# Optimization experiments

Measured on AMD Instinct MI355X. Metric: run time of the kernel, lower is better.

## Reference

```python
import jax, jax.numpy as jnp
import numpy as np
import math

B, A, T = 64, 23, 128          # batch, num_agents, max seq len
D, AE, S, H = 256, 32, 6, 8    # d_model, agent_encoding_dim, static_dim, heads
DK = D // H                     # 32
DM = D + AE                     # 288, MHA q/k/v dim
NEG = -1e10                     # masked_fill constant from source


def sinusoidal_pe(pos, d):
    # pos: int array [...], returns [..., d] standard transformer PE at positions pos
    half = jnp.arange(d // 2, dtype=jnp.float32)
    div = jnp.exp(-half * (math.log(10000.0) * 2.0 / d))          # [d/2]
    ang = pos[..., None].astype(jnp.float32) * div                # [..., d/2]
    return jnp.stack([jnp.sin(ang), jnp.cos(ang)], axis=-1).reshape(*pos.shape, d)


def setup_inputs() -> dict:
    key = jax.random.key(0)
    ks = jax.random.split(key, 20)
    std = 0.02
    data = jax.random.normal(ks[0], (B, A, T), jnp.float32)
    lengths = jax.random.randint(ks[1], (B, A), 0, T + 1).astype(jnp.int32)   # mask arg = lengths
    t = jnp.arange(T, dtype=jnp.int32)
    time = jnp.where(t[None, None, :] < lengths[:, :, None], t[None, None, :], -1)  # [B,A,T], -1 = pad
    static = jax.random.normal(ks[2], (B, S), jnp.float32)
    # per-agent Linear(1, D): weight [A, D], bias [A, D]
    W_embed = std * jax.random.normal(ks[3], (A, D), jnp.float32)
    b_embed = std * jax.random.normal(ks[4], (A, D), jnp.float32)
    E_var = std * jax.random.normal(ks[5], (A, AE), jnp.float32)            # VariateEncoding table
    W_static = std * jax.random.normal(ks[6], (S, D), jnp.float32)
    b_static = jnp.zeros((D,), jnp.float32)
    Wq = std * jax.random.normal(ks[7], (DM, D), jnp.float32); bq = jnp.zeros((D,), jnp.float32)
    Wk = std * jax.random.normal(ks[8], (DM, D), jnp.float32); bk = jnp.zeros((D,), jnp.float32)
    Wv = std * jax.random.normal(ks[9], (DM, D), jnp.float32); bv = jnp.zeros((D,), jnp.float32)
    Wo = std * jax.random.normal(ks[10], (D, DM), jnp.float32); bo = jnp.zeros((DM,), jnp.float32)
    Wg = std * jax.random.normal(ks[11], (DM + D, 1), jnp.float32); bg = jnp.zeros((1,), jnp.float32)
    return dict(data=data, time=time, mask=lengths, static=static,
                W_embed=W_embed, b_embed=b_embed, E_var=E_var,
                W_static=W_static, b_static=b_static,
                Wq=Wq, bq=bq, Wk=Wk, bk=bk, Wv=Wv, bv=bv, Wo=Wo, bo=bo,
                Wg=Wg, bg=bg)


def reference(data, time, mask, static, W_embed, b_embed, E_var, W_static, b_static,
              Wq, bq, Wk, bk, Wv, bv, Wo, bo, Wg, bg):
    lengths = mask                                            # [B,A] sequence lengths
    t = jnp.arange(T)
    valid = t[None, None, :] < lengths[:, :, None]            # [B,A,T] bool
    # mask_matrix[i,:len,:len]=1 double loop -> vectorized outer product
    mask4 = valid[:, :, :, None] & valid[:, :, None, :]       # [B,A,T,T]

    # per-agent Linear(1, D) loop -> batched rank-1 affine, then ReLU
    data_embeds = jax.nn.relu(data[..., None] * W_embed[None, :, None, :]
                              + b_embed[None, :, None, :])    # [B,A,T,D]

    # src_pe: sinusoidal positional encoding at (clamped) time values
    pe = sinusoidal_pe(jnp.maximum(time, 0), D)               # [B,A,T,D]
    src = data_embeds + pe

    # variate (agent-id) embedding concat -> [B,A,T,D+AE]; encoder = identity
    var = jnp.broadcast_to(E_var[None, :, None, :], (B, A, T, AE))
    memory = jnp.concatenate([src, var], axis=-1)             # [B,A,T,DM]

    # time-masked mean pool over T
    time_mask = time >= 0                                     # [B,A,T]
    memory = jnp.where(time_mask[..., None], memory, 0.0)
    counts = time_mask.sum(axis=2).astype(memory.dtype)       # [B,A]
    agentwise = memory.sum(axis=2) / (counts[..., None] + 1e-9)  # [B,A,DM]

    # custom MHA (dim='Time'): q_len = 1 per agent, keys/values over T
    q = jnp.einsum('bae,ed->bad', agentwise, Wq) + bq          # [B,A,D]
    k = jnp.einsum('bate,ed->batd', memory, Wk) + bk           # [B,A,T,D]
    v = jnp.einsum('bate,ed->batd', memory, Wv) + bv
    qh = q.reshape(B, A, H, DK)                                # [B,A,H,DK] (q_len=1 squeezed)
    kh = k.reshape(B, A, T, H, DK).transpose(0, 1, 3, 2, 4)    # [B,A,H,T,DK]
    vh = v.reshape(B, A, T, H, DK).transpose(0, 1, 3, 2, 4)
    scores = jnp.einsum('bahd,bahtd->baht', qh, kh) / math.sqrt(DK)  # [B,A,H,T]
    amask = mask4[:, :, 0, :]                                  # [B,A,T] row 0 of per-agent mask
    scores = jnp.where(amask[:, :, None, :], scores, NEG)
    p = jax.nn.softmax(scores, axis=-1)                        # dropout = eval (identity)
    ctx = jnp.einsum('baht,bahtd->bahd', p, vh).reshape(B, A, D)
    agent_feat = jnp.einsum('bad,de->bae', ctx, Wo) + bo       # [B,A,DM]

    # agent-masked mean pool over agents
    agent_mask = counts > 0                                    # [B,A]
    agent_feat = jnp.where(agent_mask[..., None], agent_feat, 0.0)
    denom = agent_mask.sum(axis=1).astype(agent_feat.dtype) + 1e-9
    aggre = agent_feat.sum(axis=1) / denom[:, None]            # [B,DM]

    static_feat = static @ W_static + b_static                 # [B,D]
    all_feature = jnp.concatenate([aggre, static_feat], axis=-1)  # [B,DM+D]
    return all_feature @ Wg + bg                               # [B,1]


if __name__ == '__main__':
    out = reference(**setup_inputs())
    print(out.shape, jnp.asarray(out).dtype)
```

## Files before the change

### kernel.cpp

```cpp
#include <hip/hip_runtime.h>
#include <math.h>

#define NB 64
#define NA 23
#define NT 128
#define ND 256
#define NAE 32
#define NS 6
#define NH 8
#define NDM 288

#define OFF_PEK    0
#define OFF_PECUM  32768
#define OFF_WKT    65536
#define OFF_VWO    131072
#define OFF_PEMV   133120
#define OFF_EVA    134144
#define OFF_CST    134328
#define OFF_SB     134336

__global__ __launch_bounds__(256) void setup1_kernel(
    const float* __restrict__ Wk, const float* __restrict__ Wv,
    const float* __restrict__ Wo, const float* __restrict__ Wg,
    const float* __restrict__ bv, const float* __restrict__ bo,
    const float* __restrict__ W_static, const float* __restrict__ b_static,
    const float* __restrict__ bg, const float* __restrict__ E_var,
    float* __restrict__ ws)
{
    const int blk = blockIdx.x;
    const int tid = threadIdx.x;
    float* PEcum = ws + OFF_PECUM;
    float* WkT   = ws + OFF_WKT;
    float* VWo   = ws + OFF_VWO;
    float* cst   = ws + OFF_CST;

    if (blk < 128) {
        const int g = tid >> 7, t = tid & 127;
        const int e = blk * 2 + g;
        const int i = e >> 1;
        const float kdiv = 0.07195578415606394f;
        const float dv = expf(-(float)i * kdiv);
        const float ang = (float)t * dv;
        const float v = (e & 1) ? cosf(ang) : sinf(ang);
        __shared__ float buf[256];
        buf[tid] = v;
        #pragma unroll
        for (int s = 1; s < 128; s <<= 1) {
            __syncthreads();
            float add = (t >= s) ? buf[tid - s] : 0.f;
            __syncthreads();
            buf[tid] += add;
        }
        __syncthreads();
        PEcum[t * ND + e] = buf[tid];
    } else if (blk < 384) {
        const int j = blk - 128;
        const float scale = 0.17677669529663687f;
        WkT[j * 256 + tid] = Wk[tid * ND + j] * scale;
    } else if (blk < 392) {
        const int h = blk - 384;
        __shared__ float wog[32];
        __shared__ float vext[32];
        __shared__ float vbS;
        {
            const int jj = tid >> 3, sub = tid & 7;
            const int j = h * 32 + jj;
            float acc = 0.f;
            const int m0 = sub * 36;
            #pragma unroll 4
            for (int m = m0; m < m0 + 36; ++m)
                acc = fmaf(Wo[j * NDM + m], Wg[m], acc);
            acc += __shfl_down(acc, 4, 8);
            acc += __shfl_down(acc, 2, 8);
            acc += __shfl_down(acc, 1, 8);
            if (sub == 0) wog[jj] = acc;
        }
        __syncthreads();
        {
            float acc = 0.f;
            #pragma unroll 8
            for (int jj = 0; jj < 32; ++jj)
                acc = fmaf(Wv[tid * ND + h * 32 + jj], wog[jj], acc);
            VWo[h * 256 + tid] = acc;
        }
        if (tid < 32) {
            float acc = 0.f;
            #pragma unroll 8
            for (int jj = 0; jj < 32; ++jj)
                acc = fmaf(Wv[(256 + tid) * ND + h * 32 + jj], wog[jj], acc);
            vext[tid] = acc;
        }
        if (tid == 0) {
            float acc = 0.f;
            #pragma unroll 8
            for (int jj = 0; jj < 32; ++jj)
                acc = fmaf(bv[h * 32 + jj], wog[jj], acc);
            vbS = acc;
        }
        __syncthreads();
        if (tid < NA) {
            float acc = vbS;
            #pragma unroll 8
            for (int ee = 0; ee < 32; ++ee)
                acc = fmaf(E_var[tid * NAE + ee], vext[ee], acc);
            ws[OFF_EVA + tid * NH + h] = acc;
        }
    } else {
        const int i = tid >> 5, sub = tid & 31;
        float acc = 0.f;
        if (i < 6) {
            for (int m = sub; m < 256; m += 32)
                acc = fmaf(W_static[i * ND + m], Wg[NDM + m], acc);
        } else if (i == 6) {
            for (int m = sub; m < 256; m += 32)
                acc = fmaf(b_static[m], Wg[NDM + m], acc);
        } else {
            for (int m = sub; m < NDM; m += 32)
                acc = fmaf(bo[m], Wg[m], acc);
        }
        #pragma unroll
        for (int off = 16; off > 0; off >>= 1)
            acc += __shfl_down(acc, off, 32);
        if (sub == 0) cst[i] = (i == 6) ? acc + bg[0] : acc;
    }
}

__global__ __launch_bounds__(256) void setup2_kernel(
    const float* __restrict__ Wk, float* __restrict__ ws)
{
    const int t = blockIdx.x;
    const int tid = threadIdx.x;
    __shared__ float peS[256];
    {
        const int i = tid >> 1;
        const float kdiv = 0.07195578415606394f;
        const float dv = expf(-(float)i * kdiv);
        const float ang = (float)t * dv;
        peS[tid] = (tid & 1) ? cosf(ang) : sinf(ang);
    }
    __syncthreads();
    {
        float a0 = 0.f, a1 = 0.f, a2 = 0.f, a3 = 0.f;
        #pragma unroll 4
        for (int e = 0; e < 256; e += 4) {
            a0 = fmaf(peS[e],     Wk[ e      * ND + tid], a0);
            a1 = fmaf(peS[e + 1], Wk[(e + 1) * ND + tid], a1);
            a2 = fmaf(peS[e + 2], Wk[(e + 2) * ND + tid], a2);
            a3 = fmaf(peS[e + 3], Wk[(e + 3) * ND + tid], a3);
        }
        const float scale = 0.17677669529663687f;
        ws[OFF_PEK + tid * NT + t] = ((a0 + a1) + (a2 + a3)) * scale;
    }
    {
        const int h = tid >> 5, ee = tid & 31;
        const float* vw = ws + OFF_VWO + h * 256;
        float v = 0.f;
        #pragma unroll
        for (int k = 0; k < 8; ++k)
            v = fmaf(peS[ee + 32 * k], vw[ee + 32 * k], v);
        v += __shfl_down(v, 16, 32);
        v += __shfl_down(v, 8, 32);
        v += __shfl_down(v, 4, 32);
        v += __shfl_down(v, 2, 32);
        v += __shfl_down(v, 1, 32);
        if (ee == 0) ws[OFF_PEMV + h * NT + t] = v;
    }
    if (t == 0 && tid < NB) ws[OFF_SB + tid] = 0.f;
}

#define E_ITER(KCNT) do {                                                    \
    const int e = ebase + ee;                                                \
    const int r = (e + (e >> 6)) & 3;                                        \
    const float2 wb = Wb[half][e + (e >> 6)];                                \
    const float4 cq = comboV[e * 4 + (hh ^ r)];                              \
    const float4 cm = comboV[e * 4 + ((2 | hh) ^ r)];                        \
    const float m0 = fmaxf(fmaf(xt0, wb.x, wb.y), 0.f);                      \
    aS[0][0]=fmaf(m0,cq.x,aS[0][0]); aS[0][1]=fmaf(m0,cq.y,aS[0][1]);        \
    aS[0][2]=fmaf(m0,cq.z,aS[0][2]); aS[0][3]=fmaf(m0,cq.w,aS[0][3]);        \
    aM[0][0]=fmaf(m0,cm.x,aM[0][0]); aM[0][1]=fmaf(m0,cm.y,aM[0][1]);        \
    aM[0][2]=fmaf(m0,cm.z,aM[0][2]); aM[0][3]=fmaf(m0,cm.w,aM[0][3]);        \
    const float m1 = fmaxf(fmaf(xt1, wb.x, wb.y), 0.f);                      \
    aS[1][0]=fmaf(m1,cq.x,aS[1][0]); aS[1][1]=fmaf(m1,cq.y,aS[1][1]);        \
    aS[1][2]=fmaf(m1,cq.z,aS[1][2]); aS[1][3]=fmaf(m1,cq.w,aS[1][3]);        \
    aM[1][0]=fmaf(m1,cm.x,aM[1][0]); aM[1][1]=fmaf(m1,cm.y,aM[1][1]);        \
    aM[1][2]=fmaf(m1,cm.z,aM[1][2]); aM[1][3]=fmaf(m1,cm.w,aM[1][3]);        \
    if ((KCNT) == 4) {                                                       \
        const float m2 = fmaxf(fmaf(xt2, wb.x, wb.y), 0.f);                  \
        aS[2][0]=fmaf(m2,cq.x,aS[2][0]); aS[2][1]=fmaf(m2,cq.y,aS[2][1]);    \
        aS[2][2]=fmaf(m2,cq.z,aS[2][2]); aS[2][3]=fmaf(m2,cq.w,aS[2][3]);    \
        aM[2][0]=fmaf(m2,cm.x,aM[2][0]); aM[2][1]=fmaf(m2,cm.y,aM[2][1]);    \
        aM[2][2]=fmaf(m2,cm.z,aM[2][2]); aM[2][3]=fmaf(m2,cm.w,aM[2][3]);    \
        const float m3 = fmaxf(fmaf(xt3, wb.x, wb.y), 0.f);                  \
        aS[3][0]=fmaf(m3,cq.x,aS[3][0]); aS[3][1]=fmaf(m3,cq.y,aS[3][1]);    \
        aS[3][2]=fmaf(m3,cq.z,aS[3][2]); aS[3][3]=fmaf(m3,cq.w,aS[3][3]);    \
        aM[3][0]=fmaf(m3,cm.x,aM[3][0]); aM[3][1]=fmaf(m3,cm.y,aM[3][1]);    \
        aM[3][2]=fmaf(m3,cm.z,aM[3][2]); aM[3][3]=fmaf(m3,cm.w,aM[3][3]);    \
    }                                                                        \
} while (0)

__global__ __launch_bounds__(512) void main_kernel(
    const float* __restrict__ data, const int* __restrict__ lengths,
    const float* __restrict__ W_embed, const float* __restrict__ b_embed,
    const float* __restrict__ E_var,
    const float* __restrict__ Wq, const float* __restrict__ bq,
    float* __restrict__ ws)
{
    const int pair = blockIdx.x;
    const int tid  = threadIdx.x;
    const int half = tid >> 8;
    const int lt   = tid & 255;
    const int wgh  = pair * 2 + half;
    const int ah   = wgh % NA;
    const int bh   = wgh / NA;
    const int Lh   = lengths[wgh];

    __shared__ __align__(16) float xs[2][NT];
    __shared__ __align__(16) float qs[2][ND];
    __shared__ float2 Wb[2][ND + 4];
    __shared__ __align__(16) float combo[2][ND * 16];
    __shared__ float red[2][4];

    const float* PEcum = ws + OFF_PECUM;
    const float* WkT   = ws + OFF_WKT;
    const float* VWo   = ws + OFF_VWO;
    const float* cstp  = ws + OFF_CST;
    float* agA = &combo[1][0];

    if (lt < NT) xs[half][lt] = data[wgh * NT + lt];
    __syncthreads();
    {
        const int e = lt;
        if (Lh > 0) {
            const float We = W_embed[ah * ND + e];
            const float be = b_embed[ah * ND + e];
            Wb[half][e + (e >> 6)] = make_float2(We, be);
            const float4* x4 = (const float4*)xs[half];
            float s0 = 0.f, s1 = 0.f, s2 = 0.f, s3 = 0.f;
            const int nq = Lh >> 2;
            for (int q = 0; q < nq; ++q) {
                const float4 xv = x4[q];
                s0 += fmaxf(fmaf(xv.x, We, be), 0.f);
                s1 += fmaxf(fmaf(xv.y, We, be), 0.f);
                s2 += fmaxf(fmaf(xv.z, We, be), 0.f);
                s3 += fmaxf(fmaf(xv.w, We, be), 0.f);
            }
            for (int t = nq * 4; t < Lh; ++t)
                s0 += fmaxf(fmaf(xs[half][t], We, be), 0.f);
            agA[half * NDM + e] = (((s0 + s1) + (s2 + s3)) + PEcum[(Lh - 1) * ND + e]) / (float)Lh;
        } else {
            Wb[half][e + (e >> 6)] = make_float2(0.f, 0.f);
            agA[half * NDM + e] = 0.f;
        }
    }
    if (lt < NAE) agA[half * NDM + ND + lt] = (Lh > 0) ? E_var[ah * NAE + lt] : 0.f;
    __syncthreads();

    {
        const int j = lt;
        const float4* a40 = (const float4*)(agA);
        const float4* a41 = (const float4*)(agA + NDM);
        const int fi0 = half * 36;
        float c0 = 0.f, c1 = 0.f, c2 = 0.f, c3 = 0.f;
        #pragma unroll 4
        for (int fi = fi0; fi < fi0 + 36; ++fi) {
            const float4 av0 = a40[fi];
            const float4 av1 = a41[fi];
            const int f = fi * 4;
            const float w0 = Wq[ f      * ND + j];
            const float w1 = Wq[(f + 1) * ND + j];
            const float w2 = Wq[(f + 2) * ND + j];
            const float w3 = Wq[(f + 3) * ND + j];
            c0 = fmaf(av0.x, w0, c0); c2 = fmaf(av0.y, w1, c2);
            c0 = fmaf(av0.z, w2, c0); c2 = fmaf(av0.w, w3, c2);
            c1 = fmaf(av1.x, w0, c1); c3 = fmaf(av1.y, w1, c3);
            c1 = fmaf(av1.z, w2, c1); c3 = fmaf(av1.w, w3, c3);
        }
        float* Csc = &combo[0][0];
        Csc[half * 512 +       j] = c0 + c2;
        Csc[half * 512 + 256 + j] = c1 + c3;
    }
    __syncthreads();
    {
        const float* Csc = &combo[0][0];
        qs[half][lt] = bq[lt] + Csc[half * 256 + lt] + Csc[512 + half * 256 + lt];
    }
    __syncthreads();

    {
        const int e = lt;
        const int hb = half;
        const float* wr = WkT + (hb * 128) * 256 + e;
        const float4* q40 = (const float4*)(qs[0] + hb * 128);
        const float4* q41 = (const float4*)(qs[1] + hb * 128);
        float qk0[4], qk1[4];
        #pragma unroll
        for (int h4 = 0; h4 < 4; ++h4) {
            float c00 = 0.f, c01 = 0.f, c10 = 0.f, c11 = 0.f;
            #pragma unroll
            for (int jq = 0; jq < 8; ++jq) {
                const float4 q0 = q40[h4 * 8 + jq];
                const float4 q1 = q41[h4 * 8 + jq];
                const float w0 = wr[(h4 * 32 + jq * 4 + 0) * 256];
                const float w1 = wr[(h4 * 32 + jq * 4 + 1) * 256];
                const float w2 = wr[(h4 * 32 + jq * 4 + 2) * 256];
                const float w3 = wr[(h4 * 32 + jq * 4 + 3) * 256];
                c00 = fmaf(w0, q0.x, c00); c01 = fmaf(w1, q0.y, c01);
                c00 = fmaf(w2, q0.z, c00); c01 = fmaf(w3, q0.w, c01);
                c10 = fmaf(w0, q1.x, c10); c11 = fmaf(w1, q1.y, c11);
                c10 = fmaf(w2, q1.z, c10); c11 = fmaf(w3, q1.w, c11);
            }
            qk0[h4] = c00 + c01;
            qk1[h4] = c10 + c11;
        }
        const int r = (e + (e >> 6)) & 3;
        float4* row0 = (float4*)(&combo[0][0]) + e * 4;
        float4* row1 = (float4*)(&combo[1][0]) + e * 4;
        row0[hb ^ r] = make_float4(qk0[0], qk0[1], qk0[2], qk0[3]);
        row1[hb ^ r] = make_float4(qk1[0], qk1[1], qk1[2], qk1[3]);
        const float4 vw = make_float4(VWo[(hb * 4 + 0) * 256 + e],
                                      VWo[(hb * 4 + 1) * 256 + e],
                                      VWo[(hb * 4 + 2) * 256 + e],
                                      VWo[(hb * 4 + 3) * 256 + e]);
        row0[(2 | hb) ^ r] = vw;
        row1[(2 | hb) ^ r] = vw;
    }
    __syncthreads();

    {
        const int lane = lt & 63;
        const int wv   = lt >> 6;
        const int hh   = wv & 1;
        const int tw   = wv >> 1;
        const int t0   = lane & 15;
        const int c    = lane >> 4;
        const int tb   = tw * 16 + t0;
        const int ebase = c * 64;
        const float4* comboV = (const float4*)(&combo[half][0]);
        float aS[4][4], aM[4][4];
        #pragma unroll
        for (int k = 0; k < 4; ++k)
            #pragma unroll
            for (int j = 0; j < 4; ++j) { aS[k][j] = 0.f; aM[k][j] = 0.f; }
        const float xt0 = xs[half][tb];
        const float xt1 = xs[half][tb + 32];
        const float xt2 = xs[half][tb + 64];
        const float xt3 = xs[half][tb + 96];
        if (Lh > 64) {
            #pragma unroll 4
            for (int ee = 0; ee < 64; ++ee) E_ITER(4);
        } else if (Lh > 0) {
            #pragma unroll 4
            for (int ee = 0; ee < 64; ++ee) E_ITER(2);
        }
        #pragma unroll
        for (int k = 0; k < 4; ++k)
            #pragma unroll
            for (int j = 0; j < 4; ++j) {
                float vS = aS[k][j], vM = aM[k][j];
                vS += __shfl_down(vS, 32, 64);
                vS += __shfl_down(vS, 16, 64);
                vM += __shfl_down(vM, 32, 64);
                vM += __shfl_down(vM, 16, 64);
                aS[k][j] = vS; aM[k][j] = vM;
            }
        __syncthreads();
        float* scF = &combo[half][0];
        float* mvF = scF + 1024;
        if (c == 0) {
            #pragma unroll
            for (int k = 0; k < 4; ++k)
                #pragma unroll
                for (int j = 0; j < 4; ++j) {
                    const int h = hh * 4 + j;
                    scF[h * NT + tb + 32 * k] = aS[k][j];
                    mvF[h * NT + tb + 32 * k] = aM[k][j];
                }
        }
    }
    __syncthreads();

    {
        const int h  = tid >> 6;
        const int tq = tid & 63;
        const float* pekt = ws + OFF_PEK;
        const float4* qs40 = (const float4*)(qs[0] + h * 32);
        const float4* qs41 = (const float4*)(qs[1] + h * 32);
        float b00 = 0.f, b01 = 0.f, b10 = 0.f, b11 = 0.f;
        #pragma unroll
        for (int jq = 0; jq < 8; ++jq) {
            const float4 q0 = qs40[jq];
            const float4 q1 = qs41[jq];
            const float* pr = pekt + (h * 32 + jq * 4) * NT + tq;
            const float p00 = pr[0];          const float p01 = pr[64];
            const float p10 = pr[NT];         const float p11 = pr[NT + 64];
            const float p20 = pr[2 * NT];     const float p21 = pr[2 * NT + 64];
            const float p30 = pr[3 * NT];     const float p31 = pr[3 * NT + 64];
            b00 = fmaf(q0.x, p00, b00); b00 = fmaf(q0.y, p10, b00);
            b00 = fmaf(q0.z, p20, b00); b00 = fmaf(q0.w, p30, b00);
            b01 = fmaf(q0.x, p01, b01); b01 = fmaf(q0.y, p11, b01);
            b01 = fmaf(q0.z, p21, b01); b01 = fmaf(q0.w, p31, b01);
            b10 = fmaf(q1.x, p00, b10); b10 = fmaf(q1.y, p10, b10);
            b10 = fmaf(q1.z, p20, b10); b10 = fmaf(q1.w, p30, b10);
            b11 = fmaf(q1.x, p01, b11); b11 = fmaf(q1.y, p11, b11);
            b11 = fmaf(q1.z, p21, b11); b11 = fmaf(q1.w, p31, b11);
        }
        combo[0][2048 + h * NT + tq]      = b00;
        combo[0][2048 + h * NT + tq + 64] = b01;
        combo[1][2048 + h * NT + tq]      = b10;
        combo[1][2048 + h * NT + tq + 64] = b11;
    }
    __syncthreads();

    if (Lh > 0) {
        const float* sc   = &combo[half][0];
        const float* mvb  = sc + 1024;
        const float* qkxp = sc + 2048;
        const float* pemv = ws + OFF_PEMV;
        const int wv = lt >> 6, lane = lt & 63;
        float wsum = 0.f;
        for (int hh2 = 0; hh2 < 2; ++hh2) {
            const int h = wv * 2 + hh2;
            float s1 = (lane < Lh) ? sc[h * NT + lane] + qkxp[h * NT + lane] : -3e38f;
            float s2 = (lane + 64 < Lh) ? sc[h * NT + 64 + lane] + qkxp[h * NT + 64 + lane] : -3e38f;
            float mx = fmaxf(s1, s2);
            #pragma unroll
            for (int off = 32; off > 0; off >>= 1)
                mx = fmaxf(mx, __shfl_down(mx, off, 64));
            mx = __shfl(mx, 0, 64);
            const float vbv = ws[OFF_EVA + ah * NH + h];
            float e1 = (lane < Lh) ? __expf(s1 - mx) : 0.f;
            float e2 = (lane + 64 < Lh) ? __expf(s2 - mx) : 0.f;
            float num = e1 * (mvb[h * NT + lane] + pemv[h * NT + lane] + vbv);
            num = fmaf(e2, mvb[h * NT + 64 + lane] + pemv[h * NT + 64 + lane] + vbv, num);
            float den = e1 + e2;
            #pragma unroll
            for (int off = 32; off > 0; off >>= 1) {
                num += __shfl_down(num, off, 64);
                den += __shfl_down(den, off, 64);
            }
            if (lane == 0) wsum += num / den;
        }
        if (lane == 0) red[half][wv] = wsum;
    }
    __syncthreads();
    if (lt == 0 && Lh > 0)
        atomicAdd(ws + OFF_SB + bh,
                  cstp[7] + red[half][0] + red[half][1] + red[half][2] + red[half][3]);
}

__global__ __launch_bounds__(64) void final_kernel(
    const float* __restrict__ statics, const int* __restrict__ lengths,
    const float* __restrict__ ws, float* __restrict__ out)
{
    const int b = threadIdx.x;
    const float* cst = ws + OFF_CST;
    int n = 0;
    for (int a = 0; a < NA; ++a)
        if (lengths[b * NA + a] > 0) ++n;
    float o = ws[OFF_SB + b] / ((float)n + 1e-9f);
    #pragma unroll
    for (int i = 0; i < NS; ++i)
        o = fmaf(statics[b * NS + i], cst[i], o);
    o += cst[6];
    out[b] = o;
}

extern "C" void kernel_launch(void* const* d_in, const int* in_sizes, int n_in,
                              void* d_out, int out_size, void* d_ws, size_t ws_size,
                              hipStream_t stream) {
    const float* data     = (const float*)d_in[0];
    const int*   mask     = (const int*)d_in[2];
    const float* statics  = (const float*)d_in[3];
    const float* W_embed  = (const float*)d_in[4];
    const float* b_embed  = (const float*)d_in[5];
    const float* E_var    = (const float*)d_in[6];
    const float* W_static = (const float*)d_in[7];
    const float* b_static = (const float*)d_in[8];
    const float* Wq       = (const float*)d_in[9];
    const float* bq       = (const float*)d_in[10];
    const float* Wk       = (const float*)d_in[11];
    const float* Wv       = (const float*)d_in[13];
    const float* bv       = (const float*)d_in[14];
    const float* Wo       = (const float*)d_in[15];
    const float* bo       = (const float*)d_in[16];
    const float* Wg       = (const float*)d_in[17];
    const float* bg       = (const float*)d_in[18];
    float* out = (float*)d_out;
    float* ws  = (float*)d_ws;

    setup1_kernel<<<dim3(393), dim3(256), 0, stream>>>(Wk, Wv, Wo, Wg, bv, bo,
                                                       W_static, b_static, bg, E_var, ws);
    setup2_kernel<<<dim3(128), dim3(256), 0, stream>>>(Wk, ws);
    main_kernel<<<dim3(NB * NA / 2), dim3(512), 0, stream>>>(data, mask, W_embed, b_embed,
                                                             E_var, Wq, bq, ws);
    final_kernel<<<dim3(1), dim3(64), 0, stream>>>(statics, mask, ws, out);
}
```

Before: 151.4 us.

## Fold setup2 and final kernels into setup and main to cut launches

Moves the PE·Wk and PE·VWo projections into the transpose and VWo blocks of the first setup kernel, recomputing sin/cos per block, so the second setup kernel is removed. The final reduction kernel is replaced by a last-block-done pattern: an atomic counter in the workspace picks the last main-kernel block, which computes the output. This removes two kernel launches and their serialization gaps. In exchange it adds redundant transcendental work in setup blocks and an extra atomic plus fence per main block.

```diff
diff --git a/kernel.cpp b/kernel.cpp
--- a/kernel.cpp
+++ b/kernel.cpp
@@ -9,6 +9,7 @@
 #define NS 6
 #define NH 8
 #define NDM 288
+#define NPAIR 736
 
 #define OFF_PEK    0
 #define OFF_PECUM  32768
@@ -18,8 +19,9 @@
 #define OFF_EVA    134144
 #define OFF_CST    134328
 #define OFF_SB     134336
-
-__global__ __launch_bounds__(256) void setup1_kernel(
+#define OFF_CNT    134400
+
+__global__ __launch_bounds__(256) void setup_kernel(
     const float* __restrict__ Wk, const float* __restrict__ Wv,
     const float* __restrict__ Wo, const float* __restrict__ Wg,
     const float* __restrict__ bv, const float* __restrict__ bo,
@@ -29,6 +31,7 @@
 {
     const int blk = blockIdx.x;
     const int tid = threadIdx.x;
+    const float kdiv = 0.07195578415606394f;
     float* PEcum = ws + OFF_PECUM;
     float* WkT   = ws + OFF_WKT;
     float* VWo   = ws + OFF_VWO;
@@ -38,7 +41,6 @@
         const int g = tid >> 7, t = tid & 127;
         const int e = blk * 2 + g;
         const int i = e >> 1;
-        const float kdiv = 0.07195578415606394f;
         const float dv = expf(-(float)i * kdiv);
         const float ang = (float)t * dv;
         const float v = (e & 1) ? cosf(ang) : sinf(ang);
@@ -56,12 +58,36 @@
     } else if (blk < 384) {
         const int j = blk - 128;
         const float scale = 0.17677669529663687f;
-        WkT[j * 256 + tid] = Wk[tid * ND + j] * scale;
+        __shared__ float wkS[256];
+        __shared__ float dvS[128];
+        __shared__ float pp[256];
+        const float w = Wk[tid * ND + j] * scale;
+        WkT[j * 256 + tid] = w;
+        wkS[tid] = w;
+        if (tid < 128) dvS[tid] = expf(-(float)tid * kdiv);
+        __syncthreads();
+        {
+            const int t = tid & 127, eh = tid >> 7;
+            const float tf = (float)t;
+            float acc = 0.f;
+            const int i0 = eh * 64;
+            for (int i = i0; i < i0 + 64; ++i) {
+                const float ang = tf * dvS[i];
+                acc = fmaf(sinf(ang), wkS[2 * i],     acc);
+                acc = fmaf(cosf(ang), wkS[2 * i + 1], acc);
+            }
+            pp[tid] = acc;
+        }
+        __syncthreads();
+        if (tid < 128) ws[OFF_PEK + j * NT + tid] = pp[tid] + pp[128 + tid];
     } else if (blk < 392) {
         const int h = blk - 384;
         __shared__ float wog[32];
         __shared__ float vext[32];
         __shared__ float vbS;
+        __shared__ float vS[256];
+        __shared__ float dvS2[128];
+        __shared__ float pp2[256];
         {
             const int jj = tid >> 3, sub = tid & 7;
             const int j = h * 32 + jj;
@@ -82,15 +108,18 @@
             for (int jj = 0; jj < 32; ++jj)
                 acc = fmaf(Wv[tid * ND + h * 32 + jj], wog[jj], acc);
             VWo[h * 256 + tid] = acc;
-        }
-        if (tid < 32) {
+            vS[tid] = acc;
+        }
+        if (tid < 128) dvS2[tid] = expf(-(float)tid * kdiv);
+        if (tid >= 128 && tid < 160) {
+            const int ee = tid - 128;
             float acc = 0.f;
             #pragma unroll 8
             for (int jj = 0; jj < 32; ++jj)
-                acc = fmaf(Wv[(256 + tid) * ND + h * 32 + jj], wog[jj], acc);
-            vext[tid] = acc;
-        }
-        if (tid == 0) {
+                acc = fmaf(Wv[(256 + ee) * ND + h * 32 + jj], wog[jj], acc);
+            vext[ee] = acc;
+        }
+        if (tid == 160) {
             float acc = 0.f;
             #pragma unroll 8
             for (int jj = 0; jj < 32; ++jj)
@@ -105,7 +134,23 @@
                 acc = fmaf(E_var[tid * NAE + ee], vext[ee], acc);
             ws[OFF_EVA + tid * NH + h] = acc;
         }
+        {
+            const int t = tid & 127, eh = tid >> 7;
+            const float tf = (float)t;
+            float acc = 0.f;
+            const int i0 = eh * 64;
+            for (int i = i0; i < i0 + 64; ++i) {
+                const float ang = tf * dvS2[i];
+                acc = fmaf(sinf(ang), vS[2 * i],     acc);
+                acc = fmaf(cosf(ang), vS[2 * i + 1], acc);
+            }
+            pp2[tid] = acc;
+        }
+        __syncthreads();
+        if (tid < 128) ws[OFF_PEMV + h * NT + tid] = pp2[tid] + pp2[128 + tid];
     } else {
+        if (tid < NB) ws[OFF_SB + tid] = 0.f;
+        if (tid == NB) ws[OFF_CNT] = 0.f;
         const int i = tid >> 5, sub = tid & 31;
         float acc = 0.f;
         if (i < 6) {
@@ -123,49 +168,6 @@
             acc += __shfl_down(acc, off, 32);
         if (sub == 0) cst[i] = (i == 6) ? acc + bg[0] : acc;
     }
-}
-
-__global__ __launch_bounds__(256) void setup2_kernel(
-    const float* __restrict__ Wk, float* __restrict__ ws)
-{
-    const int t = blockIdx.x;
-    const int tid = threadIdx.x;
-    __shared__ float peS[256];
-    {
-        const int i = tid >> 1;
-        const float kdiv = 0.07195578415606394f;
-        const float dv = expf(-(float)i * kdiv);
-        const float ang = (float)t * dv;
-        peS[tid] = (tid & 1) ? cosf(ang) : sinf(ang);
-    }
-    __syncthreads();
-    {
-        float a0 = 0.f, a1 = 0.f, a2 = 0.f, a3 = 0.f;
-        #pragma unroll 4
-        for (int e = 0; e < 256; e += 4) {
-            a0 = fmaf(peS[e],     Wk[ e      * ND + tid], a0);
-            a1 = fmaf(peS[e + 1], Wk[(e + 1) * ND + tid], a1);
-            a2 = fmaf(peS[e + 2], Wk[(e + 2) * ND + tid], a2);
-            a3 = fmaf(peS[e + 3], Wk[(e + 3) * ND + tid], a3);
-        }
-        const float scale = 0.17677669529663687f;
-        ws[OFF_PEK + tid * NT + t] = ((a0 + a1) + (a2 + a3)) * scale;
-    }
-    {
-        const int h = tid >> 5, ee = tid & 31;
-        const float* vw = ws + OFF_VWO + h * 256;
-        float v = 0.f;
-        #pragma unroll
-        for (int k = 0; k < 8; ++k)
-            v = fmaf(peS[ee + 32 * k], vw[ee + 32 * k], v);
-        v += __shfl_down(v, 16, 32);
-        v += __shfl_down(v, 8, 32);
-        v += __shfl_down(v, 4, 32);
-        v += __shfl_down(v, 2, 32);
-        v += __shfl_down(v, 1, 32);
-        if (ee == 0) ws[OFF_PEMV + h * NT + t] = v;
-    }
-    if (t == 0 && tid < NB) ws[OFF_SB + tid] = 0.f;
 }
 
 #define E_ITER(KCNT) do {                                                    \
@@ -203,6 +205,7 @@
     const float* __restrict__ W_embed, const float* __restrict__ b_embed,
     const float* __restrict__ E_var,
     const float* __restrict__ Wq, const float* __restrict__ bq,
+    const float* __restrict__ statics, float* __restrict__ out,
     float* __restrict__ ws)
 {
     const int pair = blockIdx.x;
@@ -219,6 +222,7 @@
     __shared__ float2 Wb[2][ND + 4];
     __shared__ __align__(16) float combo[2][ND * 16];
     __shared__ float red[2][4];
+    __shared__ int lastFin;
 
     const float* PEcum = ws + OFF_PECUM;
     const float* WkT   = ws + OFF_WKT;
@@ -443,26 +447,31 @@
         if (lane == 0) red[half][wv] = wsum;
     }
     __syncthreads();
-    if (lt == 0 && Lh > 0)
-        atomicAdd(ws + OFF_SB + bh,
-                  cstp[7] + red[half][0] + red[half][1] + red[half][2] + red[half][3]);
-}
-
-__global__ __launch_bounds__(64) void final_kernel(
-    const float* __restrict__ statics, const int* __restrict__ lengths,
-    const float* __restrict__ ws, float* __restrict__ out)
-{
-    const int b = threadIdx.x;
-    const float* cst = ws + OFF_CST;
-    int n = 0;
-    for (int a = 0; a < NA; ++a)
-        if (lengths[b * NA + a] > 0) ++n;
-    float o = ws[OFF_SB + b] / ((float)n + 1e-9f);
-    #pragma unroll
-    for (int i = 0; i < NS; ++i)
-        o = fmaf(statics[b * NS + i], cst[i], o);
-    o += cst[6];
-    out[b] = o;
+    if (lt == 0) {
+        if (Lh > 0)
+            atomicAdd(ws + OFF_SB + bh,
+                      cstp[7] + red[half][0] + red[half][1] + red[half][2] + red[half][3]);
+        __threadfence();
+    }
+    __syncthreads();
+    if (tid == 0) {
+        const int prev = atomicAdd((int*)(ws + OFF_CNT), 1);
+        lastFin = (prev == NPAIR - 1) ? 1 : 0;
+    }
+    __syncthreads();
+    if (lastFin && tid < NB) {
+        const int b = tid;
+        const float sum = atomicAdd(ws + OFF_SB + b, 0.f);
+        int n = 0;
+        for (int a = 0; a < NA; ++a)
+            if (lengths[b * NA + a] > 0) ++n;
+        float o = sum / ((float)n + 1e-9f);
+        #pragma unroll
+        for (int i = 0; i < NS; ++i)
+            o = fmaf(statics[b * NS + i], cstp[i], o);
+        o += cstp[6];
+        out[b] = o;
+    }
 }
 
 extern "C" void kernel_launch(void* const* d_in, const int* in_sizes, int n_in,
@@ -488,10 +497,8 @@
     float* out = (float*)d_out;
     float* ws  = (float*)d_ws;
 
-    setup1_kernel<<<dim3(393), dim3(256), 0, stream>>>(Wk, Wv, Wo, Wg, bv, bo,
-                                                       W_static, b_static, bg, E_var, ws);
-    setup2_kernel<<<dim3(128), dim3(256), 0, stream>>>(Wk, ws);
-    main_kernel<<<dim3(NB * NA / 2), dim3(512), 0, stream>>>(data, mask, W_embed, b_embed,
-                                                             E_var, Wq, bq, ws);
-    final_kernel<<<dim3(1), dim3(64), 0, stream>>>(statics, mask, ws, out);
+    setup_kernel<<<dim3(393), dim3(256), 0, stream>>>(Wk, Wv, Wo, Wg, bv, bo,
+                                                      W_static, b_static, bg, E_var, ws);
+    main_kernel<<<dim3(NPAIR), dim3(512), 0, stream>>>(data, mask, W_embed, b_embed,
+                                                       E_var, Wq, bq, statics, out, ws);
 }
```

Measured after the change: 171.1 us. 13.0% more time.
